# Kernel tuning notes

Hardware: AMD Instinct MI355X
Metric: run time of the kernel (lower is better)

The kernel has to match this reference:

```python
import jax, jax.numpy as jnp
import numpy as np

B, N, NFEAT, NHID, NOUT = 16, 2048, 128, 128, 64
BN_EPS = 1e-5
LRELU_ALPHA = 0.2


def setup_inputs() -> dict:
    key = jax.random.key(0)
    ks = jax.random.split(key, 6)
    stdv = 1.0 / np.sqrt(NHID)
    return {
        "x": jax.random.normal(ks[0], (B, N, NFEAT), dtype=jnp.float32),
        "adj": jnp.zeros((N, N), dtype=jnp.float32),  # passed to GAT but unused
        "adj_gcn": jax.random.uniform(ks[1], (N, N), dtype=jnp.float32),
        "gcn_weight": jax.random.uniform(ks[2], (NFEAT, NHID), minval=-stdv, maxval=stdv, dtype=jnp.float32),
        "gcn_bias": jax.random.uniform(ks[3], (NHID,), minval=-stdv, maxval=stdv, dtype=jnp.float32),
        "bn_gamma": jnp.ones((NHID,), dtype=jnp.float32),
        "bn_beta": jnp.zeros((NHID,), dtype=jnp.float32),
        "gat_W": jax.random.normal(ks[4], (NFEAT, NOUT), dtype=jnp.float32) * 0.05,
    }


def reference(x, adj, adj_gcn, gcn_weight, gcn_bias, bn_gamma, bn_beta, gat_W):
    # --- GCN layer: adj @ (x @ W) + b ---
    support = jnp.einsum("bnc,cd->bnd", x, gcn_weight)
    h = jnp.einsum("nm,bmd->bnd", adj_gcn, support) + gcn_bias  # [B,N,nhid]
    # --- BatchNorm1d (training mode: batch stats over B,N per channel) ---
    mean = h.mean(axis=(0, 1))
    var = h.var(axis=(0, 1))
    h = (h - mean) * jax.lax.rsqrt(var + BN_EPS) * bn_gamma + bn_beta
    # --- ReLU ---
    h = jax.nn.relu(h)
    # --- GAT layer (adj arg unused, as in original) ---
    h_prime = jnp.einsum("bnd,de->bne", h, gat_W)  # [B,N,nout]
    e = jnp.einsum("bne,bme->bnm", h_prime, h_prime)  # [B,N,N]
    e = jnp.where(e > 0, e, LRELU_ALPHA * e)  # LeakyReLU(0.2)
    attention = jax.nn.softmax(e, axis=1)  # softmax over dim=1 (as in source)
    # repeat-mul-sum over dim=2 reduces exactly to row-sum scaling of h_prime
    out = h_prime * attention.sum(axis=2, keepdims=True)  # [B,N,nout]
    return out
```

## Files before the change

### kernel.cpp

```cpp
#include <hip/hip_runtime.h>
#include <math.h>

#define NB 16
#define NN 2048
#define NF 128
#define NH 128
#define NO 64

typedef short bf16x8 __attribute__((ext_vector_type(8)));
typedef float f32x4 __attribute__((ext_vector_type(4)));
typedef unsigned short u16;
typedef unsigned int u32;

#define LOG2E 1.4426950408889634f
#define EXPSHIFT 43.28085122666891f

__device__ __forceinline__ u16 f2bf(float f) {
  u32 u = __builtin_bit_cast(u32, f);
  return (u16)((u + 0x7fffu + ((u >> 16) & 1u)) >> 16);
}
__device__ __forceinline__ float bf2f(u16 h) {
  u32 u = ((u32)h) << 16;
  return __builtin_bit_cast(float, u);
}

__device__ __forceinline__ void gload16(const void* g, void* l) {
  __builtin_amdgcn_global_load_lds((const __attribute__((address_space(1))) void*)g,
                                   (__attribute__((address_space(3))) void*)l, 16, 0, 0);
}
__device__ __forceinline__ f32x4 mfma16(bf16x8 a, bf16x8 b, f32x4 c) {
  return __builtin_amdgcn_mfma_f32_16x16x32_bf16(a, b, c, 0, 0, 0);
}
__device__ __forceinline__ float explr(float z) {
  return __builtin_amdgcn_exp2f(fmaf(fmaxf(z, 0.2f * z), LOG2E, -EXPSHIFT));
}

__global__ __launch_bounds__(256) void k_prep(const float* __restrict__ adj,
                                              const float* __restrict__ gcn_w,
                                              const float* __restrict__ gat_w,
                                              u16* __restrict__ adj_sw,
                                              u16* __restrict__ Wg_sw,
                                              u16* __restrict__ Wsw) {
  __shared__ u16 ts[64 * 136];
  const int t = threadIdx.x;
  const int bid = blockIdx.x;
  if (bid == 0) {
#pragma unroll
    for (int it = 0; it < 4; ++it) {
      const int s = t + it * 256;
      const int kb = s >> 6, col = s & 63;
      u16 tmp[8];
#pragma unroll
      for (int j = 0; j < 8; ++j) tmp[j] = f2bf(gat_w[(kb * 8 + j) * 64 + col]);
      uint4 o;
      o.x = (u32)tmp[0] | ((u32)tmp[1] << 16);
      o.y = (u32)tmp[2] | ((u32)tmp[3] << 16);
      o.z = (u32)tmp[4] | ((u32)tmp[5] << 16);
      o.w = (u32)tmp[6] | ((u32)tmp[7] << 16);
      *(uint4*)&Wg_sw[(size_t)s * 8] = o;
    }
  } else if (bid < 9) {
    const int s = (bid - 1) * 256 + t;
    const int kb = s >> 7, d = s & 127;
    u16 tmp[8];
#pragma unroll
    for (int j = 0; j < 8; ++j) tmp[j] = f2bf(gcn_w[(kb * 8 + j) * 128 + d]);
    uint4 o;
    o.x = (u32)tmp[0] | ((u32)tmp[1] << 16);
    o.y = (u32)tmp[2] | ((u32)tmp[3] << 16);
    o.z = (u32)tmp[4] | ((u32)tmp[5] << 16);
    o.w = (u32)tmp[6] | ((u32)tmp[7] << 16);
    *(uint4*)&Wsw[(size_t)s * 8] = o;
  } else {
    const int tile = bid - 9;
    const int n0 = (tile >> 5) * 64, m0 = (tile & 31) * 64;
#pragma unroll
    for (int k = 0; k < 4; ++k) {
      const int s = t + k * 256;
      const int row = s >> 4, c4 = (s & 15) * 4;
      const float4 f = *(const float4*)&adj[(size_t)(n0 + row) * 2048 + m0 + c4];
      uint2 pk;
      pk.x = (u32)f2bf(f.x) | ((u32)f2bf(f.y) << 16);
      pk.y = (u32)f2bf(f.z) | ((u32)f2bf(f.w) << 16);
      *(uint2*)&ts[row * 136 + c4] = pk;
    }
    __syncthreads();
#pragma unroll
    for (int k = 0; k < 2; ++k) {
      const int s = t + k * 256;
      const int kb = s >> 6, row = s & 63;
      const uint4 v = *(const uint4*)&ts[row * 136 + kb * 8];
      *(uint4*)&adj_sw[(size_t)tile * 4096 + (size_t)s * 8] = v;
    }
  }
}

__global__ __launch_bounds__(256) void k_support(const float* __restrict__ x,
                                                 const u16* __restrict__ Wsw,
                                                 u16* __restrict__ suppT_sw) {
  const int m0g = blockIdx.x * 128;
  const int t = threadIdx.x, w = t >> 6, l = t & 63;
  const int lg = l >> 4, lr = l & 15;
  __shared__ __align__(16) u16 ts[128 * 136];
  __shared__ __align__(16) u16 Bs[16384];
#pragma unroll
  for (int i = 0; i < 8; ++i) {
    const int s0 = i * 256 + w * 64;
    gload16(Wsw + (size_t)(s0 + l) * 8, &Bs[(size_t)s0 * 8]);
  }
#pragma unroll
  for (int k = 0; k < 16; ++k) {
    const int s = t + k * 256;
    const int row = s >> 5, c4 = (s & 31) * 4;
    const float4 f = *(const float4*)&x[(size_t)(m0g + row) * 128 + c4];
    uint2 pk;
    pk.x = (u32)f2bf(f.x) | ((u32)f2bf(f.y) << 16);
    pk.y = (u32)f2bf(f.z) | ((u32)f2bf(f.w) << 16);
    *(uint2*)&ts[row * 136 + c4] = pk;
  }
  __syncthreads();
  f32x4 acc[2][8];
#pragma unroll
  for (int mf = 0; mf < 2; ++mf)
#pragma unroll
    for (int nf = 0; nf < 8; ++nf) {
      acc[mf][nf][0] = 0.f; acc[mf][nf][1] = 0.f;
      acc[mf][nf][2] = 0.f; acc[mf][nf][3] = 0.f;
    }
#pragma unroll
  for (int ks = 0; ks < 4; ++ks) {
    const int kb = ks * 4 + lg;
    const bf16x8 a0 = *(const bf16x8*)&ts[(w * 32 + lr) * 136 + kb * 8];
    const bf16x8 a1 = *(const bf16x8*)&ts[(w * 32 + 16 + lr) * 136 + kb * 8];
#pragma unroll
    for (int nf = 0; nf < 8; ++nf) {
      const bf16x8 b = *(const bf16x8*)&Bs[((size_t)kb * 128 + nf * 16 + lr) * 8];
      acc[0][nf] = mfma16(a0, b, acc[0][nf]);
      acc[1][nf] = mfma16(a1, b, acc[1][nf]);
    }
  }
  __syncthreads();
  u16* os = ts;
#pragma unroll
  for (int nf = 0; nf < 8; ++nf) {
    const int d = nf * 16 + lr;
#pragma unroll
    for (int mf = 0; mf < 2; ++mf) {
      const int mb = w * 32 + mf * 16 + lg * 4;
      const u32 p0 = (u32)f2bf(acc[mf][nf][0]) | ((u32)f2bf(acc[mf][nf][1]) << 16);
      const u32 p1 = (u32)f2bf(acc[mf][nf][2]) | ((u32)f2bf(acc[mf][nf][3]) << 16);
      *(u32*)&os[d * 136 + mb] = p0;
      *(u32*)&os[d * 136 + mb + 2] = p1;
    }
  }
  __syncthreads();
  const int b = m0g >> 11, mt0 = (m0g & 2047) >> 6;
#pragma unroll
  for (int i = 0; i < 8; ++i) {
    const int s = i * 256 + t;
    const int kt = s >> 10, kb = (s >> 7) & 7, d = s & 127;
    const uint4 v = *(const uint4*)&os[d * 136 + kt * 64 + kb * 8];
    *(uint4*)&suppT_sw[((size_t)((b * 32 + mt0 + kt) * 8 + kb)) * 1024 + (size_t)d * 8] = v;
  }
}

__global__ __launch_bounds__(512) void k_gcn(const u16* __restrict__ adj_sw,
                                             const u16* __restrict__ suppT_sw,
                                             const float* __restrict__ bias,
                                             float* __restrict__ h,
                                             float* __restrict__ psum,
                                             float* __restrict__ psq) {
  const int flat = blockIdx.y * 32 + blockIdx.x;
  const int nf2 = (flat & 7) * 64 + (flat >> 3);
  const int b = nf2 >> 5, nt = nf2 & 31;
  const int n0 = nt * 64;
  const int t = threadIdx.x;
  const int w = t >> 6, l = t & 63;
  const int wm = w >> 1, wn = w & 1;
  const int lg = l >> 4, lr = l & 15;
  __shared__ __align__(16) u16 As[2][4096];
  __shared__ __align__(16) u16 Bs[2][8192];
  __shared__ float redS[4][128], redQ[4][128];

  f32x4 acc[4];
#pragma unroll
  for (int nf = 0; nf < 4; ++nf) {
    acc[nf][0] = 0.f; acc[nf][1] = 0.f;
    acc[nf][2] = 0.f; acc[nf][3] = 0.f;
  }

#define GCN_STAGE(buf, kt)                                                        \
  {                                                                               \
    gload16(adj_sw + ((size_t)(nt * 32 + (kt))) * 4096 + (size_t)t * 8,           \
            &As[buf][t * 8]);                                                     \
    _Pragma("unroll") for (int i = 0; i < 2; ++i) {                               \
      const int s = i * 512 + t;                                                  \
      gload16(suppT_sw + ((size_t)(b * 32 + (kt))) * 8192 + (size_t)s * 8,        \
              &Bs[buf][s * 8]);                                                   \
    }                                                                             \
  }

  GCN_STAGE(0, 0);
  __syncthreads();
  for (int kt = 0; kt < 32; ++kt) {
    const int cur = kt & 1;
    if (kt + 1 < 32) GCN_STAGE(cur ^ 1, kt + 1);
#pragma unroll
    for (int kb = 0; kb < 2; ++kb) {
      const int ko = kb * 4 + lg;
      const bf16x8 a0 = *(const bf16x8*)&As[cur][(ko * 64 + wm * 16 + lr) * 8];
      const bf16x8 b0 = *(const bf16x8*)&Bs[cur][(ko * 128 + wn * 64 + lr) * 8];
      const bf16x8 b1 = *(const bf16x8*)&Bs[cur][(ko * 128 + wn * 64 + 16 + lr) * 8];
      const bf16x8 b2 = *(const bf16x8*)&Bs[cur][(ko * 128 + wn * 64 + 32 + lr) * 8];
      const bf16x8 b3 = *(const bf16x8*)&Bs[cur][(ko * 128 + wn * 64 + 48 + lr) * 8];
      acc[0] = mfma16(a0, b0, acc[0]);
      acc[1] = mfma16(a0, b1, acc[1]);
      acc[2] = mfma16(a0, b2, acc[2]);
      acc[3] = mfma16(a0, b3, acc[3]);
    }
    __syncthreads();
  }
#undef GCN_STAGE
#pragma unroll
  for (int nf = 0; nf < 4; ++nf) {
    const int d = wn * 64 + nf * 16 + lr;
    const float bv = bias[d];
    float s = 0.f, q = 0.f;
#pragma unroll
    for (int r = 0; r < 4; ++r) {
      const float v = acc[nf][r] + bv;
      const int row = n0 + wm * 16 + lg * 4 + r;
      h[((size_t)(b * NN + row)) * NH + d] = v;
      s += v;
      q = fmaf(v, v, q);
    }
    s += __shfl_xor(s, 16);
    s += __shfl_xor(s, 32);
    q += __shfl_xor(q, 16);
    q += __shfl_xor(q, 32);
    if (lg == 0) {
      redS[wm][d] = s;
      redQ[wm][d] = q;
    }
  }
  __syncthreads();
  if (t < 128) {
    const int blk = b * 32 + nt;
    psum[blk * 128 + t] = redS[0][t] + redS[1][t] + redS[2][t] + redS[3][t];
    psq[blk * 128 + t] = redQ[0][t] + redQ[1][t] + redQ[2][t] + redQ[3][t];
  }
}

__global__ __launch_bounds__(1024) void k_bnstat2(const float* __restrict__ psum,
                                                  const float* __restrict__ psq,
                                                  const float* __restrict__ gamma,
                                                  const float* __restrict__ beta,
                                                  float* __restrict__ scale,
                                                  float* __restrict__ shift) {
  const int t = threadIdx.x;
  const int d = t & 127;
  const int g = t >> 7;
  float s = 0.f, q = 0.f;
  for (int i = g; i < 512; i += 8) {
    s += psum[i * 128 + d];
    q += psq[i * 128 + d];
  }
  __shared__ float ls[8][128], lq[8][128];
  ls[g][d] = s;
  lq[g][d] = q;
  __syncthreads();
  if (t < 128) {
    s = 0.f;
    q = 0.f;
#pragma unroll
    for (int i = 0; i < 8; ++i) {
      s += ls[i][t];
      q += lq[i][t];
    }
    const float inv = 1.f / (float)(NB * NN);
    const float mean = s * inv;
    const float var = q * inv - mean * mean;
    const float sc = gamma[t] * rsqrtf(var + 1e-5f);
    scale[t] = sc;
    shift[t] = beta[t] - mean * sc;
  }
}

__global__ __launch_bounds__(256) void k_hp(const float* __restrict__ h,
                                            const float* __restrict__ scale,
                                            const float* __restrict__ shift,
                                            const u16* __restrict__ Wg_sw,
                                            u16* __restrict__ hp_sw) {
  const int row0 = blockIdx.x * 64;
  const int t = threadIdx.x, w = t >> 6, l = t & 63;
  const int lg = l >> 4, lr = l & 15;
  __shared__ __align__(16) u16 him[8192];
  __shared__ __align__(16) u16 Wg[8192];
  __shared__ __align__(16) u16 hos[64][72];
  __shared__ float scs[128], shs[128];
#pragma unroll
  for (int i = 0; i < 4; ++i) {
    const int s0 = i * 256 + w * 64;
    gload16(Wg_sw + (size_t)(s0 + l) * 8, &Wg[(size_t)s0 * 8]);
  }
  if (t < 128) {
    scs[t] = scale[t];
    shs[t] = shift[t];
  }
  __syncthreads();
#pragma unroll
  for (int k = 0; k < 4; ++k) {
    const int s = t + k * 256;
    const int row = s >> 4, kb = s & 15;
    const float4 v0 = *(const float4*)&h[(size_t)(row0 + row) * NH + kb * 8];
    const float4 v1 = *(const float4*)&h[(size_t)(row0 + row) * NH + kb * 8 + 4];
    u16 p[8];
    p[0] = f2bf(fmaxf(fmaf(v0.x, scs[kb * 8 + 0], shs[kb * 8 + 0]), 0.f));
    p[1] = f2bf(fmaxf(fmaf(v0.y, scs[kb * 8 + 1], shs[kb * 8 + 1]), 0.f));
    p[2] = f2bf(fmaxf(fmaf(v0.z, scs[kb * 8 + 2], shs[kb * 8 + 2]), 0.f));
    p[3] = f2bf(fmaxf(fmaf(v0.w, scs[kb * 8 + 3], shs[kb * 8 + 3]), 0.f));
    p[4] = f2bf(fmaxf(fmaf(v1.x, scs[kb * 8 + 4], shs[kb * 8 + 4]), 0.f));
    p[5] = f2bf(fmaxf(fmaf(v1.y, scs[kb * 8 + 5], shs[kb * 8 + 5]), 0.f));
    p[6] = f2bf(fmaxf(fmaf(v1.z, scs[kb * 8 + 6], shs[kb * 8 + 6]), 0.f));
    p[7] = f2bf(fmaxf(fmaf(v1.w, scs[kb * 8 + 7], shs[kb * 8 + 7]), 0.f));
    uint4 o;
    o.x = (u32)p[0] | ((u32)p[1] << 16);
    o.y = (u32)p[2] | ((u32)p[3] << 16);
    o.z = (u32)p[4] | ((u32)p[5] << 16);
    o.w = (u32)p[6] | ((u32)p[7] << 16);
    const int boff = (row * 256 + kb * 16) ^ ((row & 7) << 4);
    *(uint4*)&him[boff >> 1] = o;
  }
  __syncthreads();
  f32x4 acc[4];
#pragma unroll
  for (int nf = 0; nf < 4; ++nf) {
    acc[nf][0] = 0.f; acc[nf][1] = 0.f;
    acc[nf][2] = 0.f; acc[nf][3] = 0.f;
  }
#pragma unroll
  for (int kks = 0; kks < 4; ++kks) {
    const int ko = kks * 4 + lg;
    const int arow = w * 16 + lr;
    const int aoff = (arow * 256 + ko * 16) ^ ((arow & 7) << 4);
    const bf16x8 a = *(const bf16x8*)&him[aoff >> 1];
#pragma unroll
    for (int nf = 0; nf < 4; ++nf) {
      const bf16x8 bfr = *(const bf16x8*)&Wg[(ko * 64 + nf * 16 + lr) * 8];
      acc[nf] = mfma16(a, bfr, acc[nf]);
    }
  }
#pragma unroll
  for (int nf = 0; nf < 4; ++nf) {
    const int col = nf * 16 + lr;
#pragma unroll
    for (int r = 0; r < 4; ++r) {
      hos[w * 16 + lg * 4 + r][col] = f2bf(acc[nf][r]);
    }
  }
  __syncthreads();
  const size_t tbase = (size_t)blockIdx.x * 4096;
#pragma unroll
  for (int k = 0; k < 2; ++k) {
    const int s = t + k * 256;
    const int kb = s >> 6, r6 = s & 63;
    const uint2 lo = *(const uint2*)&hos[r6][kb * 8];
    const uint2 hi = *(const uint2*)&hos[r6][kb * 8 + 4];
    uint4 o;
    o.x = lo.x; o.y = lo.y; o.z = hi.x; o.w = hi.y;
    *(uint4*)&hp_sw[tbase + kb * 512 + r6 * 8] = o;
  }
}

__device__ __forceinline__ void attn_swz(int& b, int& nt, int& qtr) {
  const int flat = blockIdx.y * 512 + blockIdx.x;
  const int lf = (flat & 7) * 256 + (flat >> 3);
  b = lf >> 7;
  const int rem = lf & 127;
  qtr = rem >> 5;
  nt = rem & 31;
}

__global__ __launch_bounds__(256) void k_attnA(const u16* __restrict__ hp_sw,
                                               float* __restrict__ Dpart) {
  int b, nt, qtr;
  attn_swz(b, nt, qtr);
  const int t = threadIdx.x, w = t >> 6, l = t & 63;
  const int lg = l >> 4, lr = l & 15;
  __shared__ __align__(16) u16 Cs[2][4096];
  const u16* rbase = hp_sw + (size_t)(b * 32 + nt) * 4096;
  const int qrow = (w << 4) + lr;
  const bf16x8 bq0 = *(const bf16x8*)&rbase[(lg * 64 + qrow) * 8];
  const bf16x8 bq1 = *(const bf16x8*)&rbase[((lg + 4) * 64 + qrow) * 8];
  const u16* cb = hp_sw + (size_t)(b * 32 + qtr * 8) * 4096;
#pragma unroll
  for (int i = 0; i < 2; ++i) gload16(cb + (size_t)(i * 256 + t) * 8, &Cs[0][(i * 256 + t) * 8]);
  __syncthreads();
  float S = 0.f;
  for (int mt = 0; mt < 8; ++mt) {
    const int cur = mt & 1;
    if (mt + 1 < 8) {
#pragma unroll
      for (int i = 0; i < 2; ++i)
        gload16(cb + (size_t)(mt + 1) * 4096 + (size_t)(i * 256 + t) * 8,
                &Cs[cur ^ 1][(i * 256 + t) * 8]);
    }
#pragma unroll
    for (int mf = 0; mf < 4; ++mf) {
      const bf16x8 a0 = *(const bf16x8*)&Cs[cur][(lg * 64 + mf * 16 + lr) * 8];
      const bf16x8 a1 = *(const bf16x8*)&Cs[cur][((lg + 4) * 64 + mf * 16 + lr) * 8];
      f32x4 z;
      z[0] = 0.f; z[1] = 0.f; z[2] = 0.f; z[3] = 0.f;
      z = mfma16(a0, bq0, z);
      z = mfma16(a1, bq1, z);
      S += explr(z[0]) + explr(z[1]) + explr(z[2]) + explr(z[3]);
    }
    __syncthreads();
  }
  S += __shfl_xor(S, 16);
  S += __shfl_xor(S, 32);
  if (l < 16) Dpart[qtr * 32768 + b * NN + nt * 64 + qrow] = S;
}

__global__ __launch_bounds__(256) void k_attnB(const u16* __restrict__ hp_sw,
                                               const float* __restrict__ Dpart,
                                               float* __restrict__ Spart) {
  int b, nt, qtr;
  attn_swz(b, nt, qtr);
  const int t = threadIdx.x, w = t >> 6, l = t & 63;
  const int lg = l >> 4, lr = l & 15;
  __shared__ __align__(16) u16 Cs[2][4096];
  __shared__ float iDs[512];
  const u16* rbase = hp_sw + (size_t)(b * 32 + nt) * 4096;
  const int qrow = (w << 4) + lr;
  const bf16x8 bq0 = *(const bf16x8*)&rbase[(lg * 64 + qrow) * 8];
  const bf16x8 bq1 = *(const bf16x8*)&rbase[((lg + 4) * 64 + qrow) * 8];
  const u16* cb = hp_sw + (size_t)(b * 32 + qtr * 8) * 4096;
#pragma unroll
  for (int i = 0; i < 2; ++i) gload16(cb + (size_t)(i * 256 + t) * 8, &Cs[0][(i * 256 + t) * 8]);
#pragma unroll
  for (int i = 0; i < 2; ++i) {
    const int idx = t + i * 256;
    const int n = b * NN + qtr * 512 + idx;
    iDs[idx] = 1.f / (Dpart[n] + Dpart[32768 + n] + Dpart[65536 + n] + Dpart[98304 + n]);
  }
  __syncthreads();
  float S = 0.f;
  for (int mt = 0; mt < 8; ++mt) {
    const int cur = mt & 1;
    if (mt + 1 < 8) {
#pragma unroll
      for (int i = 0; i < 2; ++i)
        gload16(cb + (size_t)(mt + 1) * 4096 + (size_t)(i * 256 + t) * 8,
                &Cs[cur ^ 1][(i * 256 + t) * 8]);
    }
#pragma unroll
    for (int mf = 0; mf < 4; ++mf) {
      const bf16x8 a0 = *(const bf16x8*)&Cs[cur][(lg * 64 + mf * 16 + lr) * 8];
      const bf16x8 a1 = *(const bf16x8*)&Cs[cur][((lg + 4) * 64 + mf * 16 + lr) * 8];
      f32x4 z;
      z[0] = 0.f; z[1] = 0.f; z[2] = 0.f; z[3] = 0.f;
      z = mfma16(a0, bq0, z);
      z = mfma16(a1, bq1, z);
      const float4 dv = *(const float4*)&iDs[mt * 64 + mf * 16 + lg * 4];
      S = fmaf(explr(z[0]), dv.x, S);
      S = fmaf(explr(z[1]), dv.y, S);
      S = fmaf(explr(z[2]), dv.z, S);
      S = fmaf(explr(z[3]), dv.w, S);
    }
    __syncthreads();
  }
  S += __shfl_xor(S, 16);
  S += __shfl_xor(S, 32);
  if (l < 16) Spart[qtr * 32768 + b * NN + nt * 64 + qrow] = S;
}

__global__ __launch_bounds__(256) void k_scale(const u16* __restrict__ hp_sw,
                                               const float* __restrict__ Spart,
                                               float* __restrict__ out) {
  const int bx = blockIdx.x;
  const int b = bx >> 5, nt = bx & 31;
  const int t = threadIdx.x;
  __shared__ float Sv[64];
  if (t < 64) {
    const int n = b * NN + nt * 64 + t;
    Sv[t] = Spart[n] + Spart[32768 + n] + Spart[65536 + n] + Spart[98304 + n];
  }
  __syncthreads();
  const u16* rbase = hp_sw + (size_t)(b * 32 + nt) * 4096;
  const int row = t >> 2;
  const float sc = Sv[row];
  const size_t R = (size_t)b * NN + nt * 64 + row;
#pragma unroll
  for (int hh = 0; hh < 2; ++hh) {
    const int kb = (t & 3) * 2 + hh;
    const u16* src = &rbase[(kb * 64 + row) * 8];
    float4 o0, o1;
    o0.x = bf2f(src[0]) * sc;
    o0.y = bf2f(src[1]) * sc;
    o0.z = bf2f(src[2]) * sc;
    o0.w = bf2f(src[3]) * sc;
    o1.x = bf2f(src[4]) * sc;
    o1.y = bf2f(src[5]) * sc;
    o1.z = bf2f(src[6]) * sc;
    o1.w = bf2f(src[7]) * sc;
    *(float4*)&out[R * NO + kb * 8] = o0;
    *(float4*)&out[R * NO + kb * 8 + 4] = o1;
  }
}

extern "C" void kernel_launch(void* const* d_in, const int* in_sizes, int n_in,
                              void* d_out, int out_size, void* d_ws, size_t ws_size,
                              hipStream_t stream) {
  const float* x = (const float*)d_in[0];
  const float* adj_gcn = (const float*)d_in[2];
  const float* gcn_w = (const float*)d_in[3];
  const float* gcn_b = (const float*)d_in[4];
  const float* gamma = (const float*)d_in[5];
  const float* beta = (const float*)d_in[6];
  const float* gat_w = (const float*)d_in[7];
  float* out = (float*)d_out;
  float* ws = (float*)d_ws;

  u16* adj_sw = (u16*)ws;
  u16* suppT_sw = (u16*)(ws + 2097152);
  float* hbuf = ws + 4194304;
  u16* hp_sw = (u16*)(ws + 8388608);
  float* psum = ws + 9437184;
  float* psq = psum + 65536;
  float* scale = psq + 65536;
  float* shift = scale + 128;
  u16* Wg_sw = (u16*)(shift + 128);
  u16* Wsw = (u16*)(shift + 128 + 4096);
  float* Dpart = ws + 9617664;
  float* Spart = Dpart + 131072;

  k_prep<<<dim3(1033), dim3(256), 0, stream>>>(adj_gcn, gcn_w, gat_w, adj_sw, Wg_sw, Wsw);
  k_support<<<dim3(256), dim3(256), 0, stream>>>(x, Wsw, suppT_sw);
  k_gcn<<<dim3(32, 16), dim3(512), 0, stream>>>(adj_sw, suppT_sw, gcn_b, hbuf, psum, psq);
  k_bnstat2<<<dim3(1), dim3(1024), 0, stream>>>(psum, psq, gamma, beta, scale, shift);
  k_hp<<<dim3(512), dim3(256), 0, stream>>>(hbuf, scale, shift, Wg_sw, hp_sw);
  k_attnA<<<dim3(512, 4), dim3(256), 0, stream>>>(hp_sw, Dpart);
  k_attnB<<<dim3(512, 4), dim3(256), 0, stream>>>(hp_sw, Dpart, Spart);
  k_scale<<<dim3(512), dim3(256), 0, stream>>>(hp_sw, Spart, out);
}
```

Measured before the change: 113.0 us.

## Fuse support GEMM into prep, BN stats and output scaling via last-block counters

Merges the support GEMM into the prep kernel as extra blocks of 64 rows, each converting the GCN weight to bf16 in LDS itself. The single-block BN statistics kernel and the final scale kernel are folded into k_gcn and k_attnB, using atomic counters so the last-arriving block does the reduction or the output write. This removes three kernel launches and their serialization gaps. In exchange it adds a memset, atomics and threadfences, and each support block redundantly converts the weight matrix.

```diff
diff --git a/kernel.cpp b/kernel.cpp
--- a/kernel.cpp
+++ b/kernel.cpp
@@ -35,13 +35,15 @@
   return __builtin_amdgcn_exp2f(fmaf(fmaxf(z, 0.2f * z), LOG2E, -EXPSHIFT));
 }
 
-__global__ __launch_bounds__(256) void k_prep(const float* __restrict__ adj,
+__global__ __launch_bounds__(256) void k_prep(const float* __restrict__ x,
+                                              const float* __restrict__ adj,
                                               const float* __restrict__ gcn_w,
                                               const float* __restrict__ gat_w,
+                                              u16* __restrict__ suppT_sw,
                                               u16* __restrict__ adj_sw,
-                                              u16* __restrict__ Wg_sw,
-                                              u16* __restrict__ Wsw) {
-  __shared__ u16 ts[64 * 136];
+                                              u16* __restrict__ Wg_sw) {
+  __shared__ __align__(16) u16 ts[64 * 136];
+  __shared__ __align__(16) u16 Bs[16384];
   const int t = threadIdx.x;
   const int bid = blockIdx.x;
   if (bid == 0) {
@@ -59,20 +61,8 @@
       o.w = (u32)tmp[6] | ((u32)tmp[7] << 16);
       *(uint4*)&Wg_sw[(size_t)s * 8] = o;
     }
-  } else if (bid < 9) {
-    const int s = (bid - 1) * 256 + t;
-    const int kb = s >> 7, d = s & 127;
-    u16 tmp[8];
-#pragma unroll
-    for (int j = 0; j < 8; ++j) tmp[j] = f2bf(gcn_w[(kb * 8 + j) * 128 + d]);
-    uint4 o;
-    o.x = (u32)tmp[0] | ((u32)tmp[1] << 16);
-    o.y = (u32)tmp[2] | ((u32)tmp[3] << 16);
-    o.z = (u32)tmp[4] | ((u32)tmp[5] << 16);
-    o.w = (u32)tmp[6] | ((u32)tmp[7] << 16);
-    *(uint4*)&Wsw[(size_t)s * 8] = o;
-  } else {
-    const int tile = bid - 9;
+  } else if (bid < 1025) {
+    const int tile = bid - 1;
     const int n0 = (tile >> 5) * 64, m0 = (tile & 31) * 64;
 #pragma unroll
     for (int k = 0; k < 4; ++k) {
@@ -92,84 +82,86 @@
       const uint4 v = *(const uint4*)&ts[row * 136 + kb * 8];
       *(uint4*)&adj_sw[(size_t)tile * 4096 + (size_t)s * 8] = v;
     }
-  }
-}
-
-__global__ __launch_bounds__(256) void k_support(const float* __restrict__ x,
-                                                 const u16* __restrict__ Wsw,
-                                                 u16* __restrict__ suppT_sw) {
-  const int m0g = blockIdx.x * 128;
-  const int t = threadIdx.x, w = t >> 6, l = t & 63;
-  const int lg = l >> 4, lr = l & 15;
-  __shared__ __align__(16) u16 ts[128 * 136];
-  __shared__ __align__(16) u16 Bs[16384];
-#pragma unroll
-  for (int i = 0; i < 8; ++i) {
-    const int s0 = i * 256 + w * 64;
-    gload16(Wsw + (size_t)(s0 + l) * 8, &Bs[(size_t)s0 * 8]);
-  }
-#pragma unroll
-  for (int k = 0; k < 16; ++k) {
-    const int s = t + k * 256;
-    const int row = s >> 5, c4 = (s & 31) * 4;
-    const float4 f = *(const float4*)&x[(size_t)(m0g + row) * 128 + c4];
-    uint2 pk;
-    pk.x = (u32)f2bf(f.x) | ((u32)f2bf(f.y) << 16);
-    pk.y = (u32)f2bf(f.z) | ((u32)f2bf(f.w) << 16);
-    *(uint2*)&ts[row * 136 + c4] = pk;
-  }
-  __syncthreads();
-  f32x4 acc[2][8];
-#pragma unroll
-  for (int mf = 0; mf < 2; ++mf)
+  } else {
+    const int sb = bid - 1025;
+    const int m0g = sb * 64;
+    const int w = t >> 6, l = t & 63;
+    const int lg = l >> 4, lr = l & 15;
+#pragma unroll
+    for (int i = 0; i < 8; ++i) {
+      const int s = t + i * 256;
+      const int kb = s >> 7, d = s & 127;
+      u16 tmp[8];
+#pragma unroll
+      for (int j = 0; j < 8; ++j) tmp[j] = f2bf(gcn_w[(kb * 8 + j) * 128 + d]);
+      uint4 o;
+      o.x = (u32)tmp[0] | ((u32)tmp[1] << 16);
+      o.y = (u32)tmp[2] | ((u32)tmp[3] << 16);
+      o.z = (u32)tmp[4] | ((u32)tmp[5] << 16);
+      o.w = (u32)tmp[6] | ((u32)tmp[7] << 16);
+      *(uint4*)&Bs[(size_t)s * 8] = o;
+    }
+#pragma unroll
+    for (int k = 0; k < 8; ++k) {
+      const int s = t + k * 256;
+      const int row = s >> 5, c4 = (s & 31) * 4;
+      const float4 f = *(const float4*)&x[(size_t)(m0g + row) * 128 + c4];
+      uint2 pk;
+      pk.x = (u32)f2bf(f.x) | ((u32)f2bf(f.y) << 16);
+      pk.y = (u32)f2bf(f.z) | ((u32)f2bf(f.w) << 16);
+      *(uint2*)&ts[row * 136 + c4] = pk;
+    }
+    __syncthreads();
+    f32x4 acc[8];
 #pragma unroll
     for (int nf = 0; nf < 8; ++nf) {
-      acc[mf][nf][0] = 0.f; acc[mf][nf][1] = 0.f;
-      acc[mf][nf][2] = 0.f; acc[mf][nf][3] = 0.f;
-    }
-#pragma unroll
-  for (int ks = 0; ks < 4; ++ks) {
-    const int kb = ks * 4 + lg;
-    const bf16x8 a0 = *(const bf16x8*)&ts[(w * 32 + lr) * 136 + kb * 8];
-    const bf16x8 a1 = *(const bf16x8*)&ts[(w * 32 + 16 + lr) * 136 + kb * 8];
+      acc[nf][0] = 0.f; acc[nf][1] = 0.f;
+      acc[nf][2] = 0.f; acc[nf][3] = 0.f;
+    }
+#pragma unroll
+    for (int ks = 0; ks < 4; ++ks) {
+      const int kb = ks * 4 + lg;
+      const bf16x8 a = *(const bf16x8*)&ts[(w * 16 + lr) * 136 + kb * 8];
+#pragma unroll
+      for (int nf = 0; nf < 8; ++nf) {
+        const bf16x8 bb = *(const bf16x8*)&Bs[((size_t)kb * 128 + nf * 16 + lr) * 8];
+        acc[nf] = mfma16(a, bb, acc[nf]);
+      }
+    }
+    __syncthreads();
+    u16* os = Bs;
 #pragma unroll
     for (int nf = 0; nf < 8; ++nf) {
-      const bf16x8 b = *(const bf16x8*)&Bs[((size_t)kb * 128 + nf * 16 + lr) * 8];
-      acc[0][nf] = mfma16(a0, b, acc[0][nf]);
-      acc[1][nf] = mfma16(a1, b, acc[1][nf]);
-    }
-  }
-  __syncthreads();
-  u16* os = ts;
-#pragma unroll
-  for (int nf = 0; nf < 8; ++nf) {
-    const int d = nf * 16 + lr;
-#pragma unroll
-    for (int mf = 0; mf < 2; ++mf) {
-      const int mb = w * 32 + mf * 16 + lg * 4;
-      const u32 p0 = (u32)f2bf(acc[mf][nf][0]) | ((u32)f2bf(acc[mf][nf][1]) << 16);
-      const u32 p1 = (u32)f2bf(acc[mf][nf][2]) | ((u32)f2bf(acc[mf][nf][3]) << 16);
-      *(u32*)&os[d * 136 + mb] = p0;
-      *(u32*)&os[d * 136 + mb + 2] = p1;
-    }
-  }
-  __syncthreads();
-  const int b = m0g >> 11, mt0 = (m0g & 2047) >> 6;
-#pragma unroll
-  for (int i = 0; i < 8; ++i) {
-    const int s = i * 256 + t;
-    const int kt = s >> 10, kb = (s >> 7) & 7, d = s & 127;
-    const uint4 v = *(const uint4*)&os[d * 136 + kt * 64 + kb * 8];
-    *(uint4*)&suppT_sw[((size_t)((b * 32 + mt0 + kt) * 8 + kb)) * 1024 + (size_t)d * 8] = v;
+      const int d = nf * 16 + lr;
+      const int mb = w * 16 + lg * 4;
+      const u32 p0 = (u32)f2bf(acc[nf][0]) | ((u32)f2bf(acc[nf][1]) << 16);
+      const u32 p1 = (u32)f2bf(acc[nf][2]) | ((u32)f2bf(acc[nf][3]) << 16);
+      *(u32*)&os[d * 72 + mb] = p0;
+      *(u32*)&os[d * 72 + mb + 2] = p1;
+    }
+    __syncthreads();
+    const int b = m0g >> 11, mt = (m0g & 2047) >> 6;
+#pragma unroll
+    for (int i = 0; i < 4; ++i) {
+      const int s = i * 256 + t;
+      const int kb = s >> 7, d = s & 127;
+      const uint4 v = *(const uint4*)&os[d * 72 + kb * 8];
+      *(uint4*)&suppT_sw[((size_t)((b * 32 + mt) * 8 + kb)) * 1024 + (size_t)d * 8] = v;
+    }
   }
 }
 
 __global__ __launch_bounds__(512) void k_gcn(const u16* __restrict__ adj_sw,
                                              const u16* __restrict__ suppT_sw,
                                              const float* __restrict__ bias,
+                                             const float* __restrict__ gamma,
+                                             const float* __restrict__ beta,
                                              float* __restrict__ h,
                                              float* __restrict__ psum,
-                                             float* __restrict__ psq) {
+                                             float* __restrict__ psq,
+                                             float* __restrict__ scale,
+                                             float* __restrict__ shift,
+                                             int* __restrict__ cnt) {
   const int flat = blockIdx.y * 32 + blockIdx.x;
   const int nf2 = (flat & 7) * 64 + (flat >> 3);
   const int b = nf2 >> 5, nt = nf2 & 31;
@@ -181,6 +173,7 @@
   __shared__ __align__(16) u16 As[2][4096];
   __shared__ __align__(16) u16 Bs[2][8192];
   __shared__ float redS[4][128], redQ[4][128];
+  __shared__ int lastS;
 
   f32x4 acc[4];
 #pragma unroll
@@ -249,40 +242,31 @@
     psum[blk * 128 + t] = redS[0][t] + redS[1][t] + redS[2][t] + redS[3][t];
     psq[blk * 128 + t] = redQ[0][t] + redQ[1][t] + redQ[2][t] + redQ[3][t];
   }
-}
-
-__global__ __launch_bounds__(1024) void k_bnstat2(const float* __restrict__ psum,
-                                                  const float* __restrict__ psq,
-                                                  const float* __restrict__ gamma,
-                                                  const float* __restrict__ beta,
-                                                  float* __restrict__ scale,
-                                                  float* __restrict__ shift) {
-  const int t = threadIdx.x;
-  const int d = t & 127;
-  const int g = t >> 7;
-  float s = 0.f, q = 0.f;
-  for (int i = g; i < 512; i += 8) {
-    s += psum[i * 128 + d];
-    q += psq[i * 128 + d];
-  }
-  __shared__ float ls[8][128], lq[8][128];
-  ls[g][d] = s;
-  lq[g][d] = q;
-  __syncthreads();
-  if (t < 128) {
-    s = 0.f;
-    q = 0.f;
-#pragma unroll
-    for (int i = 0; i < 8; ++i) {
-      s += ls[i][t];
-      q += lq[i][t];
-    }
-    const float inv = 1.f / (float)(NB * NN);
-    const float mean = s * inv;
-    const float var = q * inv - mean * mean;
-    const float sc = gamma[t] * rsqrtf(var + 1e-5f);
-    scale[t] = sc;
-    shift[t] = beta[t] - mean * sc;
+  __threadfence();
+  __syncthreads();
+  if (t == 0) lastS = (atomicAdd(cnt, 1) == 511);
+  __syncthreads();
+  if (lastS) {
+    __threadfence();
+    const int d = t & 127, g = t >> 7;
+    float s = 0.f, q = 0.f;
+    for (int i = g; i < 512; i += 4) {
+      s += psum[i * 128 + d];
+      q += psq[i * 128 + d];
+    }
+    redS[g][d] = s;
+    redQ[g][d] = q;
+    __syncthreads();
+    if (t < 128) {
+      s = redS[0][t] + redS[1][t] + redS[2][t] + redS[3][t];
+      q = redQ[0][t] + redQ[1][t] + redQ[2][t] + redQ[3][t];
+      const float inv = 1.f / (float)(NB * NN);
+      const float mean = s * inv;
+      const float var = q * inv - mean * mean;
+      const float sc = gamma[t] * rsqrtf(var + 1e-5f);
+      scale[t] = sc;
+      shift[t] = beta[t] - mean * sc;
+    }
   }
 }
 
@@ -424,13 +408,17 @@
 
 __global__ __launch_bounds__(256) void k_attnB(const u16* __restrict__ hp_sw,
                                                const float* __restrict__ Dpart,
-                                               float* __restrict__ Spart) {
+                                               float* __restrict__ Spart,
+                                               int* __restrict__ cnt2,
+                                               float* __restrict__ out) {
   int b, nt, qtr;
   attn_swz(b, nt, qtr);
   const int t = threadIdx.x, w = t >> 6, l = t & 63;
   const int lg = l >> 4, lr = l & 15;
   __shared__ __align__(16) u16 Cs[2][4096];
   __shared__ float iDs[512];
+  __shared__ float Sv[64];
+  __shared__ int lastQ;
   const u16* rbase = hp_sw + (size_t)(b * 32 + nt) * 4096;
   const int qrow = (w << 4) + lr;
   const bf16x8 bq0 = *(const bf16x8*)&rbase[(lg * 64 + qrow) * 8];
@@ -473,39 +461,36 @@
   S += __shfl_xor(S, 16);
   S += __shfl_xor(S, 32);
   if (l < 16) Spart[qtr * 32768 + b * NN + nt * 64 + qrow] = S;
-}
-
-__global__ __launch_bounds__(256) void k_scale(const u16* __restrict__ hp_sw,
-                                               const float* __restrict__ Spart,
-                                               float* __restrict__ out) {
-  const int bx = blockIdx.x;
-  const int b = bx >> 5, nt = bx & 31;
-  const int t = threadIdx.x;
-  __shared__ float Sv[64];
-  if (t < 64) {
-    const int n = b * NN + nt * 64 + t;
-    Sv[t] = Spart[n] + Spart[32768 + n] + Spart[65536 + n] + Spart[98304 + n];
-  }
-  __syncthreads();
-  const u16* rbase = hp_sw + (size_t)(b * 32 + nt) * 4096;
-  const int row = t >> 2;
-  const float sc = Sv[row];
-  const size_t R = (size_t)b * NN + nt * 64 + row;
-#pragma unroll
-  for (int hh = 0; hh < 2; ++hh) {
-    const int kb = (t & 3) * 2 + hh;
-    const u16* src = &rbase[(kb * 64 + row) * 8];
-    float4 o0, o1;
-    o0.x = bf2f(src[0]) * sc;
-    o0.y = bf2f(src[1]) * sc;
-    o0.z = bf2f(src[2]) * sc;
-    o0.w = bf2f(src[3]) * sc;
-    o1.x = bf2f(src[4]) * sc;
-    o1.y = bf2f(src[5]) * sc;
-    o1.z = bf2f(src[6]) * sc;
-    o1.w = bf2f(src[7]) * sc;
-    *(float4*)&out[R * NO + kb * 8] = o0;
-    *(float4*)&out[R * NO + kb * 8 + 4] = o1;
+  __threadfence();
+  __syncthreads();
+  if (t == 0) lastQ = (atomicAdd(&cnt2[b * 32 + nt], 1) == 3);
+  __syncthreads();
+  if (lastQ) {
+    __threadfence();
+    if (t < 64) {
+      const int n = b * NN + nt * 64 + t;
+      Sv[t] = Spart[n] + Spart[32768 + n] + Spart[65536 + n] + Spart[98304 + n];
+    }
+    __syncthreads();
+    const int row = t >> 2;
+    const float sc = Sv[row];
+    const size_t R = (size_t)b * NN + nt * 64 + row;
+#pragma unroll
+    for (int hh = 0; hh < 2; ++hh) {
+      const int kb = (t & 3) * 2 + hh;
+      const u16* src = &rbase[(kb * 64 + row) * 8];
+      float4 o0, o1;
+      o0.x = bf2f(src[0]) * sc;
+      o0.y = bf2f(src[1]) * sc;
+      o0.z = bf2f(src[2]) * sc;
+      o0.w = bf2f(src[3]) * sc;
+      o1.x = bf2f(src[4]) * sc;
+      o1.y = bf2f(src[5]) * sc;
+      o1.z = bf2f(src[6]) * sc;
+      o1.w = bf2f(src[7]) * sc;
+      *(float4*)&out[R * NO + kb * 8] = o0;
+      *(float4*)&out[R * NO + kb * 8 + 4] = o1;
+    }
   }
 }
 
@@ -531,16 +516,16 @@
   float* scale = psq + 65536;
   float* shift = scale + 128;
   u16* Wg_sw = (u16*)(shift + 128);
-  u16* Wsw = (u16*)(shift + 128 + 4096);
   float* Dpart = ws + 9617664;
   float* Spart = Dpart + 131072;
-
-  k_prep<<<dim3(1033), dim3(256), 0, stream>>>(adj_gcn, gcn_w, gat_w, adj_sw, Wg_sw, Wsw);
-  k_support<<<dim3(256), dim3(256), 0, stream>>>(x, Wsw, suppT_sw);
-  k_gcn<<<dim3(32, 16), dim3(512), 0, stream>>>(adj_sw, suppT_sw, gcn_b, hbuf, psum, psq);
-  k_bnstat2<<<dim3(1), dim3(1024), 0, stream>>>(psum, psq, gamma, beta, scale, shift);
+  int* cnt = (int*)(Spart + 131072);
+  int* cnt2 = cnt + 1;
+
+  hipMemsetAsync((void*)cnt, 0, 513 * sizeof(int), stream);
+  k_prep<<<dim3(1537), dim3(256), 0, stream>>>(x, adj_gcn, gcn_w, gat_w, suppT_sw, adj_sw, Wg_sw);
+  k_gcn<<<dim3(32, 16), dim3(512), 0, stream>>>(adj_sw, suppT_sw, gcn_b, gamma, beta, hbuf,
+                                                psum, psq, scale, shift, cnt);
   k_hp<<<dim3(512), dim3(256), 0, stream>>>(hbuf, scale, shift, Wg_sw, hp_sw);
   k_attnA<<<dim3(512, 4), dim3(256), 0, stream>>>(hp_sw, Dpart);
-  k_attnB<<<dim3(512, 4), dim3(256), 0, stream>>>(hp_sw, Dpart, Spart);
-  k_scale<<<dim3(512), dim3(256), 0, stream>>>(hp_sw, Spart, out);
-}
+  k_attnB<<<dim3(512, 4), dim3(256), 0, stream>>>(hp_sw, Dpart, Spart, cnt2, out);
+}
```

Result: slower. 393.9 us (+248.5%).
